# Kernel tuning notes

Hardware: AMD Instinct MI355X
Metric: run time of the kernel (lower is better)

Reference implementation:

```python
import jax, jax.numpy as jnp
import numpy as np
import math

NEG = -1e9


def maximum_path(logp, mask):
    # logp, mask: [B, Tx, Ty]; Viterbi-style monotonic alignment search (VITS MAS)
    B, Tx, Ty = logp.shape
    lp = jnp.where(mask > 0, logp, NEG)
    # forward DP: value[x, y] = lp[x, y] + max(value[x, y-1], value[x-1, y-1])
    v0 = jnp.where(jnp.arange(Tx)[None, :] == 0, lp[:, :, 0], NEG)  # [B, Tx]

    def fwd(v, lp_y):
        v_diag = jnp.pad(v[:, :-1], ((0, 0), (1, 0)), constant_values=NEG)
        take_diag = v_diag > v  # strict >, matches cython 'value[x,y-1] < value[x-1,y-1]'
        return lp_y + jnp.maximum(v, v_diag), take_diag

    lp_rest = jnp.moveaxis(lp[:, :, 1:], 2, 0)  # [Ty-1, B, Tx]
    _, dirs = jax.lax.scan(fwd, v0, lp_rest)
    dirs = jnp.concatenate([jnp.zeros((1, B, Tx), bool), dirs], axis=0)  # [Ty, B, Tx]

    t_x = mask[:, :, 0].sum(axis=1).astype(jnp.int32)  # valid text length per batch
    t_y = mask[:, 0, :].sum(axis=1).astype(jnp.int32)  # valid spec length per batch

    def back(idx, inp):
        dir_y, y = inp  # dir_y [B, Tx], y scalar
        active = (y < t_y)  # [B]
        row = jax.nn.one_hot(idx, Tx, dtype=logp.dtype) * active[:, None].astype(logp.dtype)
        d = jnp.take_along_axis(dir_y, idx[:, None], axis=1)[:, 0]
        idx = jnp.where(active, idx - d.astype(jnp.int32), idx)
        return idx, row

    ys = jnp.arange(Ty - 1, -1, -1)
    _, rows = jax.lax.scan(back, t_x - 1, (dirs[::-1], ys))
    path = jnp.moveaxis(rows[::-1], 0, 2)  # [B, Tx, Ty]
    return path


def _make_masks(x_lengths, y_lengths, Tx, Ty):
    x_len = jnp.clip(x_lengths, 2, Tx)
    y_len = jnp.clip(y_lengths, 2, Ty)
    y_len = jnp.maximum(y_len, x_len)  # MAS needs T_y >= T_x per sample
    x_mask = (jnp.arange(Tx)[None, :] < x_len[:, None]).astype(jnp.float32)  # [B, Tx]
    y_mask = (jnp.arange(Ty)[None, :] < y_len[:, None]).astype(jnp.float32)  # [B, Ty]
    return x_mask, y_mask


def setup_inputs() -> dict:
    key = jax.random.key(0)
    B, C, Tx, Ty = 32, 192, 512, 2048
    k1, k2, k3, k4, k5 = jax.random.split(key, 5)
    z_p = jax.random.normal(k1, (B, C, Ty), dtype=jnp.float32)
    m_p = jax.random.normal(k2, (B, C, Tx), dtype=jnp.float32)
    logs_p = jax.random.normal(k3, (B, C, Tx), dtype=jnp.float32) * 0.3
    x_lengths = jax.random.randint(k4, (B,), Tx // 2, Tx + 1, dtype=jnp.int32)
    y_lengths = jax.random.randint(k5, (B,), Ty // 2, Ty + 1, dtype=jnp.int32)
    return {"z_p": z_p, "m_p": m_p, "logs_p": logs_p, "x_lengths": x_lengths, "y_lengths": y_lengths}


def reference(z_p, m_p, logs_p, x_lengths, y_lengths):
    B, C, Ty = z_p.shape
    Tx = m_p.shape[2]
    x_mask, y_mask = _make_masks(x_lengths, y_lengths, Tx, Ty)
    attn_mask = x_mask[:, :, None] * y_mask[:, None, :]  # [B, Tx, Ty]

    # log N(z_p ; m_p, exp(logs_p)) scored for every (text, spec) pair
    o_scale = jnp.exp(-2.0 * logs_p)  # [B, C, Tx]
    logp1 = jnp.sum(-0.5 * math.log(2.0 * math.pi) - logs_p, axis=1)[:, :, None]  # [B, Tx, 1]
    logp2 = jnp.einsum('bct,bcs->bts', o_scale, -0.5 * z_p ** 2)  # [B, Tx, Ty]
    logp3 = jnp.einsum('bct,bcs->bts', m_p * o_scale, z_p)
    logp4 = jnp.sum(-0.5 * m_p ** 2 * o_scale, axis=1)[:, :, None]
    logp = logp2 + logp3 + logp1 + logp4

    attn = maximum_path(logp, attn_mask)  # [B, Tx, Ty], hard 0/1 alignment
    attn_durations = attn.sum(axis=2)[:, None, :]  # [B, 1, Tx]

    # expand text stats to spec frames: torch.einsum('klmn,kjm->kjn', attn[:,None], m_p)
    m_p_dur = jnp.einsum('bts,bct->bcs', attn, m_p)      # [B, C, Ty]
    logs_p_dur = jnp.einsum('bts,bct->bcs', attn, logs_p)
    return attn_durations, attn[:, None], m_p_dur, logs_p_dur
```

## Files before the change

kernel.cpp:

```cpp
#include <hip/hip_runtime.h>

#define NEGV -1e9f
#define BB 32
#define CC 192
#define TXD 512
#define TYD 2048

#define E_DUR   0
#define E_ATTN  16384
#define E_MP    33570816
#define E_LS    46153728
#define E_TOTAL 58736640

#define OFF_DIRS  6291456

#define WS_PATH 0ull
#define WS_YST  131072ull
#define WS_TXTY 196864ull
#define WS_NEED 262144ull

typedef _Float16 f16x8 __attribute__((ext_vector_type(8)));
typedef float f32x4 __attribute__((ext_vector_type(4)));

__device__ __forceinline__ void glds16(const void* g, void* l) {
    __builtin_amdgcn_global_load_lds((const __attribute__((address_space(1))) unsigned*)g,
                                     (__attribute__((address_space(3))) unsigned*)l, 16, 0, 0);
}
__device__ __forceinline__ unsigned packh(_Float16 a, _Float16 b) {
    union { _Float16 h[2]; unsigned u; } x; x.h[0] = a; x.h[1] = b; return x.u;
}

__global__ __launch_bounds__(256) void k_prepB(const float* __restrict__ logs_p,
                                               const float* __restrict__ m_p,
                                               const int* __restrict__ xl,
                                               const int* __restrict__ yl,
                                               _Float16* __restrict__ Bpl,
                                               float* __restrict__ l14,
                                               unsigned* __restrict__ txty) {
    __shared__ float lst[CC][33];
    __shared__ float mst[CC][33];
    __shared__ float p14[8][32];
    int b = blockIdx.y, t0 = blockIdx.x * 32, tid = threadIdx.x;
    const float* lsb = logs_p + (size_t)b * CC * TXD + t0;
    const float* mb  = m_p    + (size_t)b * CC * TXD + t0;
#pragma unroll
    for (int i = 0; i < 24; ++i) {
        int u = i * 256 + tid, c = u >> 5, t = u & 31;
        lst[c][t] = lsb[(size_t)c * TXD + t];
        mst[c][t] = mb [(size_t)c * TXD + t];
    }
    __syncthreads();
    { int q = tid >> 5, t = tid & 31; float s = 0.f;
      for (int c = q * 24; c < q * 24 + 24; ++c) {
          float ls = lst[c][t], m = mst[c][t];
          float o = expf(-2.f * ls);
          s += -0.918938533204672741780329736406f - ls - 0.5f * m * m * o;
      }
      p14[q][t] = s; }
    __syncthreads();
    if (tid < 32) {
        float s = 0.f;
#pragma unroll
        for (int q = 0; q < 8; ++q) s += p14[q][tid];
        l14[b * TXD + t0 + tid] = s;
    }
    _Float16* Bb = Bpl + (size_t)b * (4 * TXD * CC);
    unsigned* B0 = (unsigned*)(Bb);
    unsigned* B1 = (unsigned*)(Bb + (size_t)1 * TXD * CC);
    unsigned* B2 = (unsigned*)(Bb + (size_t)2 * TXD * CC);
    unsigned* B3 = (unsigned*)(Bb + (size_t)3 * TXD * CC);
#pragma unroll
    for (int i = 0; i < 12; ++i) {
        int u = i * 256 + tid, t = u / 96, cp = u - t * 96, c = cp * 2;
        float ls0 = lst[c][t], ls1 = lst[c + 1][t];
        float m0 = mst[c][t], m1 = mst[c + 1][t];
        float o0 = expf(-2.f * ls0), o1 = expf(-2.f * ls1);
        float w0 = m0 * o0, w1 = m1 * o1;
        _Float16 oh0 = (_Float16)o0, oh1 = (_Float16)o1;
        _Float16 ol0 = (_Float16)(o0 - (float)oh0), ol1 = (_Float16)(o1 - (float)oh1);
        _Float16 wh0 = (_Float16)w0, wh1 = (_Float16)w1;
        _Float16 wl0 = (_Float16)(w0 - (float)wh0), wl1 = (_Float16)(w1 - (float)wh1);
        int ui = ((t0 + t) * CC + c) >> 1;
        B0[ui] = packh(oh0, oh1);
        B1[ui] = packh(ol0, ol1);
        B2[ui] = packh(wh0, wh1);
        B3[ui] = packh(wl0, wl1);
    }
    if (blockIdx.x == 0 && blockIdx.y == 0 && tid < BB) {
        int txv = min(max(xl[tid], 2), TXD);
        int tyv = min(max(yl[tid], 2), TYD);
        tyv = max(tyv, txv);
        txty[tid] = (unsigned)txv;
        txty[BB + tid] = (unsigned)tyv;
    }
}

__global__ __launch_bounds__(256) void k_prepZ(const float* __restrict__ z_p,
                                               _Float16* __restrict__ Zpl, int sBase) {
    __shared__ float zt[CC][65];
    int b = blockIdx.y, s0 = blockIdx.x * 64, tid = threadIdx.x;
    const float* zb = z_p + (size_t)b * CC * TYD + sBase + s0;
#pragma unroll
    for (int i = 0; i < 48; ++i) {
        int u = i * 256 + tid, c = u >> 6, s = u & 63;
        zt[c][s] = zb[(size_t)c * TYD + s];
    }
    __syncthreads();
    _Float16* Zb = Zpl + (size_t)b * (4 * 1024 * CC);
    unsigned* Z0 = (unsigned*)(Zb);
    unsigned* Z1 = (unsigned*)(Zb + (size_t)1 * 1024 * CC);
    unsigned* Z2 = (unsigned*)(Zb + (size_t)2 * 1024 * CC);
    unsigned* Z3 = (unsigned*)(Zb + (size_t)3 * 1024 * CC);
#pragma unroll
    for (int i = 0; i < 24; ++i) {
        int u = i * 256 + tid, s = u / 96, cp = u - s * 96, c = cp * 2;
        float z0 = zt[c][s], z1 = zt[c + 1][s];
        float P0 = -0.5f * z0 * z0, P1 = -0.5f * z1 * z1;
        _Float16 ph0 = (_Float16)P0, ph1 = (_Float16)P1;
        _Float16 pl0 = (_Float16)(P0 - (float)ph0), pl1 = (_Float16)(P1 - (float)ph1);
        _Float16 zh0 = (_Float16)z0, zh1 = (_Float16)z1;
        _Float16 zl0 = (_Float16)(z0 - (float)zh0), zl1 = (_Float16)(z1 - (float)zh1);
        int ui = ((s0 + s) * CC + c) >> 1;
        Z0[ui] = packh(ph0, ph1);
        Z1[ui] = packh(pl0, pl1);
        Z2[ui] = packh(zh0, zh1);
        Z3[ui] = packh(zl0, zl1);
    }
}

__global__ __launch_bounds__(256, 2) void k_mm(const _Float16* __restrict__ Zpl,
                                               const _Float16* __restrict__ Bpl,
                                               const float* __restrict__ l14,
                                               const unsigned* __restrict__ txty,
                                               float* __restrict__ L, int sBase) {
    __shared__ __align__(16) char As[32768];
    __shared__ __align__(16) char Bs[16384];
    int bid = blockIdx.x;
    int xcd = bid & 7, idx = bid >> 3;
    int b = xcd + 8 * (idx >> 4);
    int tile = idx & 15;
    int s0 = (tile >> 2) * 256, t0 = (tile & 3) * 128;
    int txb = (int)txty[b], tyb = (int)txty[BB + b];
    int sg0 = sBase + s0;
    if (sg0 >= tyb) return;
    int tid = threadIdx.x, l = tid & 63, w = tid >> 6;
    float* Lt = L + ((size_t)b * TYD + sg0) * TXD + t0;
    if (t0 >= txb) {
#pragma unroll
        for (int i = 0; i < 32; ++i) {
            int u = i * 256 + tid, r = u >> 5, c4 = (u & 31) * 4;
            *(float4*)(Lt + (size_t)r * TXD + c4) = make_float4(NEGV, NEGV, NEGV, NEGV);
        }
        return;
    }
    f32x4 acc[4][8];
#pragma unroll
    for (int i = 0; i < 4; ++i)
#pragma unroll
        for (int j = 0; j < 8; ++j) acc[i][j] = (f32x4){0.f, 0.f, 0.f, 0.f};

    const char* Zb = (const char*)(Zpl + (size_t)b * (4 * 1024 * CC));
    const char* Bb = (const char*)(Bpl + (size_t)b * (4 * TXD * CC));
    int lrow = l >> 3;
    int gOff = lrow * 384 + (((l & 7) ^ lrow) * 16);
    int arow_off = (w * 64 + (l & 15)) * 128;
    int brow_off = (l & 15) * 128;
    int slot0 = (((l >> 4) + 0) ^ (l & 7)) * 16;
    int slot1 = (((l >> 4) + 4) ^ (l & 7)) * 16;

    for (int pass = 0; pass < 6; ++pass) {
        int ap = ((pass >= 3) ? 2 : 0) + ((pass == 2 || pass == 5) ? 1 : 0);
        int bp = ((pass >= 3) ? 2 : 0) + ((pass == 1 || pass == 4) ? 1 : 0);
        const char* Zp = Zb + ((size_t)ap * 1024 + s0) * 384;
        const char* Bp = Bb + ((size_t)bp * TXD + t0) * 384;
        for (int k0 = 0; k0 < 384; k0 += 128) {
            __syncthreads();
#pragma unroll
            for (int j = 0; j < 8; ++j) {
                int c = w * 8 + j;
                glds16(Zp + (size_t)c * (8 * 384) + gOff + k0, As + c * 1024);
            }
#pragma unroll
            for (int j = 0; j < 4; ++j) {
                int c = w * 4 + j;
                glds16(Bp + (size_t)c * (8 * 384) + gOff + k0, Bs + c * 1024);
            }
            __syncthreads();
#pragma unroll
            for (int ks = 0; ks < 2; ++ks) {
                int so = ks ? slot1 : slot0;
                f16x8 av[4], bv[8];
#pragma unroll
                for (int fm = 0; fm < 4; ++fm)
                    av[fm] = *(const f16x8*)(As + arow_off + fm * (16 * 128) + so);
#pragma unroll
                for (int fn = 0; fn < 8; ++fn)
                    bv[fn] = *(const f16x8*)(Bs + brow_off + fn * (16 * 128) + so);
#pragma unroll
                for (int fm = 0; fm < 4; ++fm)
#pragma unroll
                    for (int fn = 0; fn < 8; ++fn)
                        acc[fm][fn] = __builtin_amdgcn_mfma_f32_16x16x32_f16(
                            av[fm], bv[fn], acc[fm][fn], 0, 0, 0);
            }
        }
    }
    float l14v[8];
#pragma unroll
    for (int fn = 0; fn < 8; ++fn) l14v[fn] = l14[b * TXD + t0 + fn * 16 + (l & 15)];
    int sb = sg0 + w * 64 + (l >> 4) * 4;
    int tcol = t0 + (l & 15);
#pragma unroll
    for (int fm = 0; fm < 4; ++fm)
#pragma unroll
        for (int r = 0; r < 4; ++r) {
            int sg = sb + fm * 16 + r;
            bool sv = sg < tyb;
            float* Lrow = L + ((size_t)b * TYD + sg) * TXD;
#pragma unroll
            for (int fn = 0; fn < 8; ++fn) {
                int t = tcol + fn * 16;
                Lrow[t] = (sv && t < txb) ? (acc[fm][fn][r] + l14v[fn]) : NEGV;
            }
        }
}

__global__ __launch_bounds__(128) void k_dp(const float* __restrict__ L,
                                            const unsigned* __restrict__ txty,
                                            unsigned* __restrict__ dirsG,
                                            unsigned short* __restrict__ pathG,
                                            unsigned* __restrict__ ystartG,
                                            float* __restrict__ outDur) {
    __shared__ __align__(16) float ring[32 * 512];
    __shared__ unsigned char dmaps[32 * 512];
    __shared__ unsigned short path[TYD];
    __shared__ unsigned cnt[513];
    __shared__ unsigned ebuf[32];
    int b = blockIdx.x, tid = threadIdx.x;
    int lane = tid & 63, wid = tid >> 6;
    int tx = (int)txty[b], ty = (int)txty[BB + b];
    const char* Lb = (const char*)(L + (size_t)b * (TYD * TXD));
    unsigned* dGw = dirsG + (size_t)b * (512 * 64);
    int G8 = (ty + 7) >> 3;

    if (wid == 1) {
        int c0s = lane ^ ((lane >> 3) & 7);
        int srcOff0 = c0s * 16;
        int srcOff1 = srcOff0 + 1024;
        char* ringc = (char*)ring;
#define STAGE_GRP(GR) do {                                                  \
        _Pragma("unroll")                                                   \
        for (int q_ = 0; q_ < 8; ++q_) {                                    \
            int r_ = 8 * (GR) + q_;                                         \
            int rc_ = min(r_, ty - 1);                                      \
            const char* src_ = Lb + (size_t)rc_ * 2048;                     \
            char* dst_ = ringc + (size_t)(r_ & 31) * 2048;                  \
            glds16(src_ + srcOff0, dst_);                                   \
            glds16(src_ + srcOff1, dst_ + 1024);                            \
        } } while (0)
        STAGE_GRP(0); STAGE_GRP(1); STAGE_GRP(2);
        asm volatile("s_waitcnt vmcnt(16)" ::: "memory");
        __builtin_amdgcn_s_barrier();
        for (int g = 0; g < G8; ++g) {
            __builtin_amdgcn_sched_barrier(0);
            STAGE_GRP(g + 3);
            asm volatile("s_waitcnt vmcnt(16)" ::: "memory");
            __builtin_amdgcn_s_barrier();
        }
#undef STAGE_GRP
    } else {
        int sl0 = (2 * lane) ^ ((lane >> 2) & 7);
        int sl1 = sl0 ^ 1;
        const char* ringc = (const char*)ring;
        float v[8];
        unsigned p[8];
        float4 loA[8], hiA[8], loB[8], hiB[8];
#define READ_GRP(LO, HI, GN) do {                                           \
        const char* rb_ = ringc + (((GN) & 3) << 14);                       \
        _Pragma("unroll")                                                   \
        for (int q_ = 0; q_ < 8; ++q_) {                                    \
            LO[q_] = *(const float4*)(rb_ + q_ * 2048 + sl0 * 16);          \
            HI[q_] = *(const float4*)(rb_ + q_ * 2048 + sl1 * 16);          \
        } } while (0)
#define DP_GRP(LO, HI, G_) do {                                             \
        unsigned w0_ = 0, w1_ = 0;                                          \
        _Pragma("unroll")                                                   \
        for (int q_ = 0; q_ < 8; ++q_) {                                    \
            int y_ = 8 * (G_) + q_;                                         \
            if ((G_) == 0 && q_ == 0) {                                     \
                float lp_[8] = {LO[0].x, LO[0].y, LO[0].z, LO[0].w,         \
                                HI[0].x, HI[0].y, HI[0].z, HI[0].w};        \
                _Pragma("unroll")                                           \
                for (int i = 0; i < 8; ++i) {                               \
                    int x_ = lane * 8 + i;                                  \
                    v[i] = (x_ == 0) ? lp_[i] : NEGV;                       \
                    p[i] = (unsigned)x_;                                    \
                }                                                           \
            } else if (y_ < ty) {                                           \
                float cur_[8] = {LO[q_].x, LO[q_].y, LO[q_].z, LO[q_].w,    \
                                 HI[q_].x, HI[q_].y, HI[q_].z, HI[q_].w};   \
                float vp0_ = __int_as_float(__builtin_amdgcn_mov_dpp(       \
                    __float_as_int(v[7]), 0x138, 0xf, 0xf, true));          \
                unsigned pp0_ = (unsigned)__builtin_amdgcn_mov_dpp(         \
                    (int)p[7], 0x138, 0xf, 0xf, true);                      \
                if (lane == 0) vp0_ = NEGV;                                 \
                unsigned bits_ = 0;                                         \
                _Pragma("unroll")                                           \
                for (int i = 7; i >= 0; --i) {                              \
                    float vp_ = (i == 0) ? vp0_ : v[i - 1];                 \
                    unsigned pp_ = (i == 0) ? pp0_ : p[i - 1];              \
                    bool d_ = vp_ > v[i];                                   \
                    v[i] = cur_[i] + (d_ ? vp_ : v[i]);                     \
                    p[i] = d_ ? pp_ : p[i];                                 \
                    bits_ |= (d_ ? 1u : 0u) << i;                           \
                }                                                           \
                if (q_ < 4) w0_ |= bits_ << (8 * q_);                       \
                else        w1_ |= bits_ << (8 * (q_ - 4));                 \
                if (q_ == 0 && ((G_) & 7) == 0 && (G_) != 0) {              \
                    _Pragma("unroll")                                       \
                    for (int i = 0; i < 8; ++i) p[i] = (unsigned)(lane * 8 + i); \
                }                                                           \
                if (q_ == 7 && ((G_) & 7) == 7) {                           \
                    int c_ = y_ >> 6;                                       \
                    _Pragma("unroll")                                       \
                    for (int i = 0; i < 8; ++i)                             \
                        dmaps[c_ * 512 + lane * 8 + i] =                    \
                            (unsigned char)((unsigned)(lane * 8 + i) - p[i]); \
                }                                                           \
            }                                                               \
        }                                                                   \
        dGw[(2 * (G_)) * 64 + lane] = w0_;                                  \
        dGw[(2 * (G_) + 1) * 64 + lane] = w1_;                              \
        } while (0)
        __builtin_amdgcn_s_barrier();
        __builtin_amdgcn_sched_barrier(0);
        READ_GRP(loA, hiA, 0);
        for (int g = 0; g < G8;) {
            READ_GRP(loB, hiB, g + 1);
            DP_GRP(loA, hiA, g);
            ++g;
            __builtin_amdgcn_s_barrier();
            __builtin_amdgcn_sched_barrier(0);
            if (g >= G8) break;
            READ_GRP(loA, hiA, g + 1);
            DP_GRP(loB, hiB, g);
            ++g;
            __builtin_amdgcn_s_barrier();
            __builtin_amdgcn_sched_barrier(0);
        }
#undef READ_GRP
#undef DP_GRP
    }
    asm volatile("s_waitcnt vmcnt(0)" ::: "memory");
    __syncthreads();

    int c0 = (ty - 1) >> 6;
    if (tid == 0) {
        int pos = tx - 1;
        for (int y = ty - 1; y >= (c0 << 6); --y) {
            path[y] = (unsigned short)pos;
            unsigned wv = dGw[(y >> 2) * 64 + (pos >> 3)];
            pos -= (int)((wv >> (((y & 3) << 3) | (pos & 7))) & 1u);
        }
        for (int c = c0 - 1; c >= 0; --c) {
            ebuf[c] = (unsigned)pos;
            int P = pos - (int)dmaps[c * 512 + pos];
            unsigned wv = dGw[(c << 4) * 64 + (P >> 3)];
            pos = P - (int)((wv >> (P & 7)) & 1u);
        }
    }
    __syncthreads();
    if (tid < c0) {
        int c = tid;
        int pos = (int)ebuf[c];
        for (int y = (c << 6) + 63; y >= (c << 6); --y) {
            path[y] = (unsigned short)pos;
            unsigned wv = dGw[(y >> 2) * 64 + (pos >> 3)];
            pos -= (int)((wv >> (((y & 3) << 3) | (pos & 7))) & 1u);
        }
    }
    __syncthreads();

    for (int i = tid; i < 513; i += 128) cnt[i] = 0;
    __syncthreads();
    for (int y = tid; y < ty; y += 128) atomicAdd(&cnt[path[y]], 1u);
    __syncthreads();

    if (wid == 0) {
        unsigned c8[8], lsum = 0;
#pragma unroll
        for (int i = 0; i < 8; ++i) {
            c8[i] = cnt[lane * 8 + i];
            lsum += c8[i];
        }
        unsigned incl = lsum;
        for (int d = 1; d < 64; d <<= 1) {
            unsigned t = (unsigned)__shfl_up((int)incl, d);
            if (lane >= d) incl += t;
        }
        unsigned run = incl - lsum;
#pragma unroll
        for (int i = 0; i < 8; ++i) {
            int x = lane * 8 + i;
            ystartG[b * 513 + x] = run;
            outDur[(size_t)b * TXD + x] = (float)c8[i];
            run += c8[i];
        }
        if (lane == 0) ystartG[b * 513 + 512] = (unsigned)ty;
    }
    for (int y = tid; y < ty; y += 128) pathG[b * TYD + y] = path[y];
}

__global__ __launch_bounds__(64) void k_attn(const unsigned* __restrict__ ystartG,
                                             float* __restrict__ out) {
    int x = blockIdx.x, b = blockIdx.y, lane = threadIdx.x;
    unsigned s0 = ystartG[b * 513 + x];
    unsigned s1 = ystartG[b * 513 + x + 1];
    float* row = out + E_ATTN + ((size_t)(b * TXD + x)) * TYD + lane * 32;
#pragma unroll
    for (int k = 0; k < 8; ++k) {
        unsigned y0 = (unsigned)(lane * 32 + k * 4);
        float4 o;
        o.x = (y0 + 0 >= s0 && y0 + 0 < s1) ? 1.0f : 0.0f;
        o.y = (y0 + 1 >= s0 && y0 + 1 < s1) ? 1.0f : 0.0f;
        o.z = (y0 + 2 >= s0 && y0 + 2 < s1) ? 1.0f : 0.0f;
        o.w = (y0 + 3 >= s0 && y0 + 3 < s1) ? 1.0f : 0.0f;
        *(float4*)(row + k * 4) = o;
    }
}

__global__ __launch_bounds__(256) void k_gather(const float* __restrict__ m_p,
                                                const float* __restrict__ logs_p,
                                                const unsigned short* __restrict__ pathG,
                                                const unsigned* __restrict__ txty,
                                                float* __restrict__ out) {
    __shared__ unsigned short px[64];
    int yc = blockIdx.x, b = blockIdx.y;
    int y0 = yc * 64, tid = threadIdx.x;
    int lane = tid & 63, w = tid >> 6;
    int ty = (int)txty[BB + b];
    if (tid < 64) px[tid] = (y0 + tid < ty) ? pathG[b * TYD + y0 + tid] : 0;
    __syncthreads();
    bool act = (y0 + lane) < ty;
    int xx = (int)px[lane];
    for (int c = w; c < CC; c += 4) {
        float mv = act ? m_p[((size_t)b * CC + c) * TXD + xx] : 0.0f;
        float lv = act ? logs_p[((size_t)b * CC + c) * TXD + xx] : 0.0f;
        size_t oidx = ((size_t)(b * CC + c)) * TYD + y0 + lane;
        out[E_MP + oidx] = mv;
        out[E_LS + oidx] = lv;
    }
}

extern "C" void kernel_launch(void* const* d_in, const int* in_sizes, int n_in,
                              void* d_out, int out_size, void* d_ws, size_t ws_size,
                              hipStream_t stream) {
    if (out_size < E_TOTAL) return;
    if (ws_size < WS_NEED) return;
    const float* z_p    = (const float*)d_in[0];
    const float* m_p    = (const float*)d_in[1];
    const float* logs_p = (const float*)d_in[2];
    const int* xl       = (const int*)d_in[3];
    const int* yl       = (const int*)d_in[4];
    float* out = (float*)d_out;
    char* ws = (char*)d_ws;

    float* l14            = out + E_DUR;
    float* L              = out + E_ATTN;
    _Float16* Zpl         = (_Float16*)(out + E_MP);
    _Float16* Bpl         = (_Float16*)(out + E_LS);
    unsigned* dirsG       = (unsigned*)(out + E_LS + OFF_DIRS);
    unsigned short* pathG = (unsigned short*)(ws + WS_PATH);
    unsigned* ystartG     = (unsigned*)(ws + WS_YST);
    unsigned* txty        = (unsigned*)(ws + WS_TXTY);

    hipLaunchKernelGGL(k_prepB, dim3(16, BB), dim3(256), 0, stream,
                       logs_p, m_p, xl, yl, Bpl, l14, txty);
    hipLaunchKernelGGL(k_prepZ, dim3(16, BB), dim3(256), 0, stream, z_p, Zpl, 0);
    hipLaunchKernelGGL(k_mm, dim3(512), dim3(256), 0, stream, Zpl, Bpl, l14, txty, L, 0);
    hipLaunchKernelGGL(k_prepZ, dim3(16, BB), dim3(256), 0, stream, z_p, Zpl, 1024);
    hipLaunchKernelGGL(k_mm, dim3(512), dim3(256), 0, stream, Zpl, Bpl, l14, txty, L, 1024);
    hipLaunchKernelGGL(k_dp, dim3(BB), dim3(128), 0, stream, L, txty, dirsG, pathG, ystartG, out + E_DUR);
    hipLaunchKernelGGL(k_attn, dim3(TXD, BB), dim3(64), 0, stream, ystartG, out);
    hipLaunchKernelGGL(k_gather, dim3(TYD / 64, BB), dim3(256), 0, stream, m_p, logs_p, pathG, txty, out);
}
```

Measured before the change: 523.9 us.

## Replace producer/consumer LDS ring in DP kernel with single-wave register double-buffering

The DP kernel previously used a second wavefront to stage logp rows into an LDS ring via async global-to-LDS loads, with barriers each group. It now runs a single 64-lane wave that loads rows directly from global memory into two register buffers, alternating them so the loads for the next groups are in flight while the current group is processed. This removes the LDS ring, the barriers and the producer wave. The risk is that the prefetch is only about two groups deep, so global memory latency may be exposed on this serial, latency-bound recurrence.

```diff
diff --git a/kernel.cpp b/kernel.cpp
--- a/kernel.cpp
+++ b/kernel.cpp
@@ -225,63 +225,36 @@
         }
 }
 
-__global__ __launch_bounds__(128) void k_dp(const float* __restrict__ L,
-                                            const unsigned* __restrict__ txty,
-                                            unsigned* __restrict__ dirsG,
-                                            unsigned short* __restrict__ pathG,
-                                            unsigned* __restrict__ ystartG,
-                                            float* __restrict__ outDur) {
-    __shared__ __align__(16) float ring[32 * 512];
+__global__ __launch_bounds__(64) void k_dp(const float* __restrict__ L,
+                                           const unsigned* __restrict__ txty,
+                                           unsigned* __restrict__ dirsG,
+                                           unsigned short* __restrict__ pathG,
+                                           unsigned* __restrict__ ystartG,
+                                           float* __restrict__ outDur) {
     __shared__ unsigned char dmaps[32 * 512];
     __shared__ unsigned short path[TYD];
     __shared__ unsigned cnt[513];
     __shared__ unsigned ebuf[32];
-    int b = blockIdx.x, tid = threadIdx.x;
-    int lane = tid & 63, wid = tid >> 6;
+    int b = blockIdx.x, lane = threadIdx.x;
     int tx = (int)txty[b], ty = (int)txty[BB + b];
-    const char* Lb = (const char*)(L + (size_t)b * (TYD * TXD));
+    const float* Lb = L + (size_t)b * (TYD * TXD);
     unsigned* dGw = dirsG + (size_t)b * (512 * 64);
+
+    float4 aLo[8], aHi[8], bLo[8], bHi[8];
+    float v[8];
+    unsigned p[8];
     int G8 = (ty + 7) >> 3;
 
-    if (wid == 1) {
-        int c0s = lane ^ ((lane >> 3) & 7);
-        int srcOff0 = c0s * 16;
-        int srcOff1 = srcOff0 + 1024;
-        char* ringc = (char*)ring;
-#define STAGE_GRP(GR) do {                                                  \
+#define LOAD_GRP(LO, HI, GN) do {                                           \
         _Pragma("unroll")                                                   \
         for (int q_ = 0; q_ < 8; ++q_) {                                    \
-            int r_ = 8 * (GR) + q_;                                         \
-            int rc_ = min(r_, ty - 1);                                      \
-            const char* src_ = Lb + (size_t)rc_ * 2048;                     \
-            char* dst_ = ringc + (size_t)(r_ & 31) * 2048;                  \
-            glds16(src_ + srcOff0, dst_);                                   \
-            glds16(src_ + srcOff1, dst_ + 1024);                            \
+            int r_ = 8 * (GN) + q_;                                         \
+            r_ = (r_ < ty) ? r_ : (ty - 1);                                 \
+            const float* rp_ = Lb + (size_t)r_ * TXD + lane * 8;            \
+            LO[q_] = *(const float4*)(rp_);                                 \
+            HI[q_] = *(const float4*)(rp_ + 4);                             \
         } } while (0)
-        STAGE_GRP(0); STAGE_GRP(1); STAGE_GRP(2);
-        asm volatile("s_waitcnt vmcnt(16)" ::: "memory");
-        __builtin_amdgcn_s_barrier();
-        for (int g = 0; g < G8; ++g) {
-            __builtin_amdgcn_sched_barrier(0);
-            STAGE_GRP(g + 3);
-            asm volatile("s_waitcnt vmcnt(16)" ::: "memory");
-            __builtin_amdgcn_s_barrier();
-        }
-#undef STAGE_GRP
-    } else {
-        int sl0 = (2 * lane) ^ ((lane >> 2) & 7);
-        int sl1 = sl0 ^ 1;
-        const char* ringc = (const char*)ring;
-        float v[8];
-        unsigned p[8];
-        float4 loA[8], hiA[8], loB[8], hiB[8];
-#define READ_GRP(LO, HI, GN) do {                                           \
-        const char* rb_ = ringc + (((GN) & 3) << 14);                       \
-        _Pragma("unroll")                                                   \
-        for (int q_ = 0; q_ < 8; ++q_) {                                    \
-            LO[q_] = *(const float4*)(rb_ + q_ * 2048 + sl0 * 16);          \
-            HI[q_] = *(const float4*)(rb_ + q_ * 2048 + sl1 * 16);          \
-        } } while (0)
+
 #define DP_GRP(LO, HI, G_) do {                                             \
         unsigned w0_ = 0, w1_ = 0;                                          \
         _Pragma("unroll")                                                   \
@@ -332,30 +305,23 @@
         dGw[(2 * (G_)) * 64 + lane] = w0_;                                  \
         dGw[(2 * (G_) + 1) * 64 + lane] = w1_;                              \
         } while (0)
-        __builtin_amdgcn_s_barrier();
-        __builtin_amdgcn_sched_barrier(0);
-        READ_GRP(loA, hiA, 0);
-        for (int g = 0; g < G8;) {
-            READ_GRP(loB, hiB, g + 1);
-            DP_GRP(loA, hiA, g);
-            ++g;
-            __builtin_amdgcn_s_barrier();
-            __builtin_amdgcn_sched_barrier(0);
-            if (g >= G8) break;
-            READ_GRP(loA, hiA, g + 1);
-            DP_GRP(loB, hiB, g);
-            ++g;
-            __builtin_amdgcn_s_barrier();
-            __builtin_amdgcn_sched_barrier(0);
-        }
-#undef READ_GRP
+
+    LOAD_GRP(aLo, aHi, 0);
+    LOAD_GRP(bLo, bHi, 1);
+    for (int g = 0; g < G8; g += 2) {
+        DP_GRP(aLo, aHi, g);
+        LOAD_GRP(aLo, aHi, g + 2);
+        if (g + 1 < G8) {
+            DP_GRP(bLo, bHi, g + 1);
+            LOAD_GRP(bLo, bHi, g + 3);
+        }
+    }
+#undef LOAD_GRP
 #undef DP_GRP
-    }
-    asm volatile("s_waitcnt vmcnt(0)" ::: "memory");
     __syncthreads();
 
     int c0 = (ty - 1) >> 6;
-    if (tid == 0) {
+    if (lane == 0) {
         int pos = tx - 1;
         for (int y = ty - 1; y >= (c0 << 6); --y) {
             path[y] = (unsigned short)pos;
@@ -370,8 +336,8 @@
         }
     }
     __syncthreads();
-    if (tid < c0) {
-        int c = tid;
+    if (lane < c0) {
+        int c = lane;
         int pos = (int)ebuf[c];
         for (int y = (c << 6) + 63; y >= (c << 6); --y) {
             path[y] = (unsigned short)pos;
@@ -381,34 +347,32 @@
     }
     __syncthreads();
 
-    for (int i = tid; i < 513; i += 128) cnt[i] = 0;
-    __syncthreads();
-    for (int y = tid; y < ty; y += 128) atomicAdd(&cnt[path[y]], 1u);
-    __syncthreads();
-
-    if (wid == 0) {
-        unsigned c8[8], lsum = 0;
-#pragma unroll
-        for (int i = 0; i < 8; ++i) {
-            c8[i] = cnt[lane * 8 + i];
-            lsum += c8[i];
-        }
-        unsigned incl = lsum;
-        for (int d = 1; d < 64; d <<= 1) {
-            unsigned t = (unsigned)__shfl_up((int)incl, d);
-            if (lane >= d) incl += t;
-        }
-        unsigned run = incl - lsum;
-#pragma unroll
-        for (int i = 0; i < 8; ++i) {
-            int x = lane * 8 + i;
-            ystartG[b * 513 + x] = run;
-            outDur[(size_t)b * TXD + x] = (float)c8[i];
-            run += c8[i];
-        }
-        if (lane == 0) ystartG[b * 513 + 512] = (unsigned)ty;
-    }
-    for (int y = tid; y < ty; y += 128) pathG[b * TYD + y] = path[y];
+    for (int i = lane; i < 513; i += 64) cnt[i] = 0;
+    __syncthreads();
+    for (int y = lane; y < ty; y += 64) atomicAdd(&cnt[path[y]], 1u);
+    __syncthreads();
+
+    unsigned c8[8], lsum = 0;
+#pragma unroll
+    for (int i = 0; i < 8; ++i) {
+        c8[i] = cnt[lane * 8 + i];
+        lsum += c8[i];
+    }
+    unsigned incl = lsum;
+    for (int d = 1; d < 64; d <<= 1) {
+        unsigned t = (unsigned)__shfl_up((int)incl, d);
+        if (lane >= d) incl += t;
+    }
+    unsigned run = incl - lsum;
+#pragma unroll
+    for (int i = 0; i < 8; ++i) {
+        int x = lane * 8 + i;
+        ystartG[b * 513 + x] = run;
+        outDur[(size_t)b * TXD + x] = (float)c8[i];
+        run += c8[i];
+    }
+    if (lane == 0) ystartG[b * 513 + 512] = (unsigned)ty;
+    for (int y = lane; y < ty; y += 64) pathG[b * TYD + y] = path[y];
 }
 
 __global__ __launch_bounds__(64) void k_attn(const unsigned* __restrict__ ystartG,
@@ -480,7 +444,7 @@
     hipLaunchKernelGGL(k_mm, dim3(512), dim3(256), 0, stream, Zpl, Bpl, l14, txty, L, 0);
     hipLaunchKernelGGL(k_prepZ, dim3(16, BB), dim3(256), 0, stream, z_p, Zpl, 1024);
     hipLaunchKernelGGL(k_mm, dim3(512), dim3(256), 0, stream, Zpl, Bpl, l14, txty, L, 1024);
-    hipLaunchKernelGGL(k_dp, dim3(BB), dim3(128), 0, stream, L, txty, dirsG, pathG, ystartG, out + E_DUR);
+    hipLaunchKernelGGL(k_dp, dim3(BB), dim3(64), 0, stream, L, txty, dirsG, pathG, ystartG, out + E_DUR);
     hipLaunchKernelGGL(k_attn, dim3(TXD, BB), dim3(64), 0, stream, ystartG, out);
     hipLaunchKernelGGL(k_gather, dim3(TYD / 64, BB), dim3(256), 0, stream, m_p, logs_p, pathG, txty, out);
 }
```

Result: slower. 545.5 us (+4.1%).
